# Kernel optimization log

Hardware: AMD Instinct MI355X
Metric: run time of the kernel (lower is better)

Reference implementation:

```python
import jax, jax.numpy as jnp
import numpy as np

B, S, D, H, F, REF = 4, 1024, 512, 8, 2048, 2
HGRID = 32   # sqrt(seq_len)
HALF = 3     # 7x7 window -> half-width 3


def _masks():
    i = jnp.arange(HGRID)
    near = jnp.abs(i[:, None] - i[None, :]) <= HALF            # [h,h]
    inside = (near[:, None, :, None] & near[None, :, None, :]).reshape(S, S)
    # reverse=True mask (mca): outside-window -> -inf, inside -> 0
    m_rev = jnp.where(inside, 0.0, -jnp.inf).astype(jnp.float32)
    # reverse=False mask (msa/nsa): inside-window -> -inf, outside -> 0 (faithful to source)
    m_fwd = jnp.where(inside, -jnp.inf, 0.0).astype(jnp.float32)
    return m_rev, m_fwd


def _mha(q, k, v, w, b, ow, ob, mask):
    # torch nn.MultiheadAttention, batch_first, eval mode (no dropout)
    hd = D // H
    wq, wk, wv = jnp.split(w, 3, axis=0)
    bq, bk, bv = jnp.split(b, 3)

    def proj(t, wt, bt):
        Bt, Lt = t.shape[0], t.shape[1]
        return (t @ wt.T + bt).reshape(Bt, Lt, H, hd).transpose(0, 2, 1, 3)

    qh, kh, vh = proj(q, wq, bq), proj(k, wk, bk), proj(v, wv, bv)
    scores = jnp.einsum('bhqd,bhkd->bhqk', qh, kh) / jnp.sqrt(jnp.float32(hd))
    if mask is not None:
        scores = scores + mask
    a = jax.nn.softmax(scores, axis=-1)
    o = jnp.einsum('bhqk,bhkd->bhqd', a, vh).transpose(0, 2, 1, 3).reshape(q.shape[0], q.shape[1], D)
    return o @ ow.T + ob


def _ln(x, g, b, eps=1e-5):
    m = x.mean(-1, keepdims=True)
    v = ((x - m) ** 2).mean(-1, keepdims=True)
    return (x - m) / jnp.sqrt(v + eps) * g + b


def setup_inputs() -> dict:
    key = jax.random.key(0)
    ks = jax.random.split(key, 16)
    d = {}
    d['x'] = jax.random.normal(ks[0], (B, S, D), jnp.float32)
    d['ref_mca'] = jax.random.normal(ks[1], (B, REF * S, D), jnp.float32)
    d['gate'] = jax.random.uniform(ks[2], (B, S, 5), jnp.float32)
    i = 3
    for p in ['mca', 'ca', 'msa', 'nsa', 'sa']:
        d[p + '_w'] = 0.02 * jax.random.normal(ks[i], (3 * D, D), jnp.float32); i += 1
        d[p + '_b'] = jnp.zeros((3 * D,), jnp.float32)
        d[p + '_ow'] = 0.02 * jax.random.normal(ks[i], (D, D), jnp.float32); i += 1
        d[p + '_ob'] = jnp.zeros((D,), jnp.float32)
    d['ln1_g'] = jnp.ones((D,), jnp.float32); d['ln1_b'] = jnp.zeros((D,), jnp.float32)
    d['ln2_g'] = jnp.ones((D,), jnp.float32); d['ln2_b'] = jnp.zeros((D,), jnp.float32)
    d['fc1_w'] = 0.02 * jax.random.normal(ks[i], (F, D), jnp.float32); i += 1
    d['fc1_b'] = jnp.zeros((F,), jnp.float32)
    d['fc2_w'] = 0.02 * jax.random.normal(ks[i], (D, F), jnp.float32); i += 1
    d['fc2_b'] = jnp.zeros((D,), jnp.float32)
    return d


def reference(x, ref_mca, gate,
              mca_w, mca_b, mca_ow, mca_ob,
              ca_w, ca_b, ca_ow, ca_ob,
              msa_w, msa_b, msa_ow, msa_ob,
              nsa_w, nsa_b, nsa_ow, nsa_ob,
              sa_w, sa_b, sa_ow, sa_ob,
              ln1_g, ln1_b, ln2_g, ln2_b,
              fc1_w, fc1_b, fc2_w, fc2_b):
    m_rev, m_fwd = _masks()
    # mca branch: sum attention over each seq_len chunk of ref_mca (window-inside mask)
    mca_x = jnp.zeros_like(x)
    for r in range(REF):
        chunk = ref_mca[:, r * S:(r + 1) * S, :]
        mca_x = mca_x + _mha(x, chunk, chunk, mca_w, mca_b, mca_ow, mca_ob, m_rev)
    # faithful to source: loop variable leaks, so ca/nsa use the LAST chunk
    ref_last = ref_mca[:, (REF - 1) * S:, :]
    new_x = gate[:, :, 0:1] * mca_x
    new_x = new_x + gate[:, :, 1:2] * _mha(x, ref_last, ref_last, ca_w, ca_b, ca_ow, ca_ob, None)
    new_x = new_x + gate[:, :, 2:3] * _mha(x, x, x, msa_w, msa_b, msa_ow, msa_ob, m_fwd)
    new_x = new_x + gate[:, :, 3:4] * _mha(x, ref_last, x, nsa_w, nsa_b, nsa_ow, nsa_ob, m_fwd)
    new_x = new_x + gate[:, :, 4:5] * _mha(x, x, x, sa_w, sa_b, sa_ow, sa_ob, None)
    h = _ln(new_x, ln1_g, ln1_b)
    y = jax.nn.gelu(h @ fc1_w.T + fc1_b, approximate=False) @ fc2_w.T + fc2_b
    return _ln(h + y, ln2_g, ln2_b)
```

## Files before the change

### kernel.cpp

```cpp
#include <hip/hip_runtime.h>

typedef __bf16 bf16_t;
typedef bf16_t bf16x8 __attribute__((ext_vector_type(8)));
typedef float f32x4v __attribute__((ext_vector_type(4)));
typedef unsigned int u32;
typedef unsigned long long u64;

__device__ __forceinline__ void gload16(const bf16_t* g, bf16_t* l) {
    __builtin_amdgcn_global_load_lds((const __attribute__((address_space(1))) u32*)g,
                                     (__attribute__((address_space(3))) u32*)l, 16, 0, 0);
}

#define QSCALE 0.18033688011112042f

struct PackBDesc {
    int nseg;
    int blkOf[21];
    const float* src[20];
    bf16_t* dst[20];
    int chunks[20];
    int dstLd[20];
    int shift[20];
};

__global__ __launch_bounds__(256) void packb_k(PackBDesc d) {
    int b = blockIdx.x;
    int s = 0;
    while (s + 1 < d.nseg && b >= d.blkOf[s + 1]) ++s;
    int idx = (b - d.blkOf[s]) * 256 + threadIdx.x;
    if (idx >= d.chunks[s]) return;
    const float* src = d.src[s] + (size_t)idx * 8;
    int r = idx >> d.shift[s];
    int c8 = idx & ((1 << d.shift[s]) - 1);
    bf16_t* dst = d.dst[s] + (size_t)r * d.dstLd[s] + (size_t)c8 * 8;
    float4 v0 = reinterpret_cast<const float4*>(src)[0];
    float4 v1 = reinterpret_cast<const float4*>(src)[1];
    bf16x8 o;
    o[0] = (bf16_t)v0.x; o[1] = (bf16_t)v0.y; o[2] = (bf16_t)v0.z; o[3] = (bf16_t)v0.w;
    o[4] = (bf16_t)v1.x; o[5] = (bf16_t)v1.y; o[6] = (bf16_t)v1.z; o[7] = (bf16_t)v1.w;
    *reinterpret_cast<bf16x8*>(dst) = o;
}

struct PackFDesc {
    int nseg;
    int blkOf[15];
    const float* src[14];
    float* dst[14];
    int n[14];
};

__global__ __launch_bounds__(256) void packf_k(PackFDesc d) {
    int b = blockIdx.x;
    int s = 0;
    while (s + 1 < d.nseg && b >= d.blkOf[s + 1]) ++s;
    int idx = (b - d.blkOf[s]) * 256 + threadIdx.x;
    if (idx >= d.n[s]) return;
    d.dst[s][idx] = d.src[s][idx];
}

template <int EPI, int BM, int BN>
__device__ __forceinline__ void gemm_core(
    int tm, int tn, int bz,
    const bf16_t* __restrict__ A, int aBS, int aRowOff, int lda,
    const bf16_t* __restrict__ B,
    const float* __restrict__ bias,
    void* __restrict__ Out, int ldo, size_t outSplitStride,
    const float* __restrict__ gate, const float* __restrict__ obcat,
    int kStart, int kLen, u64 scaleMask) {
    constexpr int MB = BM / 32, NB = BN / 32, WM = BM / 2, WN = BN / 2;
    constexpr int CA = BM / 64, CB = BN / 64;
    __shared__ __attribute__((aligned(16))) bf16_t As[2][BM * 32];
    __shared__ __attribute__((aligned(16))) bf16_t Bs[2][BN * 32];
    const int tid = threadIdx.x, lane = tid & 63, w = tid >> 6;
    const int wm = w >> 1, wn = w & 1;
    const int l15 = lane & 15, l16 = lane >> 4;
    const int colS = (lane & 3) * 8, rowS = lane >> 2;

    auto remap = [&](int m) { return (m >> 10) * aBS + aRowOff + (m & 1023); };

    const bf16_t* aS[CA];
    const bf16_t* bS[CB];
#pragma unroll
    for (int c = 0; c < CA; ++c)
        aS[c] = A + (size_t)remap(tm * BM + (CA * w + c) * 16 + rowS) * lda + kStart + colS;
#pragma unroll
    for (int c = 0; c < CB; ++c)
        bS[c] = B + (size_t)(tn * BN + (CB * w + c) * 16 + rowS) * lda + kStart + colS;

    auto stage = [&](int buf, int t) {
        const size_t o = (size_t)t * 32;
#pragma unroll
        for (int c = 0; c < CA; ++c) gload16(aS[c] + o, &As[buf][(CA * w + c) * 512]);
#pragma unroll
        for (int c = 0; c < CB; ++c) gload16(bS[c] + o, &Bs[buf][(CB * w + c) * 512]);
    };

    f32x4v acc[MB][NB] = {};
    const int nt = kLen / 32;
    stage(0, 0);
    __syncthreads();
    int cur = 0;
    for (int t = 0; t < nt; ++t) {
        if (t + 1 < nt) stage(cur ^ 1, t + 1);
        bf16x8 af[MB], bff[NB];
#pragma unroll
        for (int mi = 0; mi < MB; ++mi)
            af[mi] = *reinterpret_cast<const bf16x8*>(&As[cur][(wm * WM + mi * 16 + l15) * 32 + l16 * 8]);
#pragma unroll
        for (int ni = 0; ni < NB; ++ni)
            bff[ni] = *reinterpret_cast<const bf16x8*>(&Bs[cur][(wn * WN + ni * 16 + l15) * 32 + l16 * 8]);
#pragma unroll
        for (int mi = 0; mi < MB; ++mi)
#pragma unroll
            for (int ni = 0; ni < NB; ++ni)
                acc[mi][ni] = __builtin_amdgcn_mfma_f32_16x16x32_bf16(af[mi], bff[ni], acc[mi][ni], 0, 0, 0);
        __syncthreads();
        cur ^= 1;
    }

    const bool doScale = (EPI == 0) && ((scaleMask >> tn) & 1ULL);
#pragma unroll
    for (int mi = 0; mi < MB; ++mi) {
#pragma unroll
        for (int ni = 0; ni < NB; ++ni) {
#pragma unroll
            for (int i = 0; i < 4; ++i) {
                int row = tm * BM + wm * WM + mi * 16 + l16 * 4 + i;
                int n = tn * BN + wn * WN + ni * 16 + l15;
                float v = acc[mi][ni][i];
                if (bias && bz == 0) v += bias[n];
                if constexpr (EPI == 0) {
                    if (doScale) v *= QSCALE;
                    ((bf16_t*)Out)[(size_t)row * ldo + n] = (bf16_t)v;
                } else if constexpr (EPI == 1) {
                    float g = 0.5f * v * (1.0f + erff(v * 0.70710678118654752f));
                    ((bf16_t*)Out)[(size_t)row * ldo + n] = (bf16_t)g;
                } else if constexpr (EPI == 3) {
                    ((float*)Out + (size_t)bz * outSplitStride)[(size_t)row * ldo + n] = v;
                } else {
                    if (obcat && bz == 0) {
#pragma unroll
                        for (int p = 0; p < 5; ++p) {
                            float c = (p == 0) ? 2.0f : 1.0f;
                            v += gate[row * 5 + p] * c * obcat[p * 512 + n];
                        }
                    }
                    ((float*)Out + (size_t)bz * outSplitStride)[(size_t)row * ldo + n] = v;
                }
            }
        }
    }
}

struct ProjDesc {
    const bf16_t* A[3];
    int aBS[3], aRowOff[3];
    const bf16_t* B[3];
    const float* bias[3];
    bf16_t* Out[3];
    int ldo[3];
    int ntn[3], base[3];
    u64 qmask[3];
};

__global__ __launch_bounds__(256) void proj_k(ProjDesc d) {
    int wg = (blockIdx.x & 7) * 272 + (blockIdx.x >> 3);
    int s = (wg >= d.base[2]) ? 2 : (wg >= d.base[1]) ? 1 : 0;
    int local = wg - d.base[s];
    int tn = local % d.ntn[s];
    int tm = local / d.ntn[s];
    gemm_core<0, 128, 128>(tm, tn, 0, d.A[s], d.aBS[s], d.aRowOff[s], 512,
                           d.B[s], d.bias[s], d.Out[s], d.ldo[s], 0, nullptr, nullptr, 0, 512,
                           d.qmask[s]);
}

template <int EPI, int BM, int BN>
__global__ __launch_bounds__(256) void gemmT(
    const bf16_t* __restrict__ A, int aBS, int aRowOff, int lda,
    const bf16_t* __restrict__ B, const float* __restrict__ bias,
    void* __restrict__ Out, int ldo, size_t outSplitStride,
    const float* __restrict__ gate, const float* __restrict__ obcat, int kPerSplit) {
    gemm_core<EPI, BM, BN>(blockIdx.y, blockIdx.x, blockIdx.z, A, aBS, aRowOff, lda, B, bias,
                           Out, ldo, outSplitStride, gate, obcat, blockIdx.z * kPerSplit, kPerSplit, 0);
}

struct AttnDesc {
    const bf16_t* Q[6];
    const bf16_t* K[6];
    const bf16_t* V[6];
    int ldq[6], ldk[6], ldv[6];
    int segOff[6], gidx[6], mask[6];
    bf16_t* acat;
    bf16_t* Op;
    float* Mp;
    float* Lp;
    const float* gate;
};

__global__ __launch_bounds__(512) void attn5_k(AttnDesc d) {
    __shared__ __attribute__((aligned(16))) bf16_t Ks[64][72];
    __shared__ __attribute__((aligned(16))) bf16_t Vt[64][72];
    __shared__ __attribute__((aligned(16))) bf16_t Ps[8][16][40];

    int bid = blockIdx.x;
    int g = bid % 320;
    int qt = bid / 320;
    int u, lg;
    if (g < 32) { u = 0; lg = g; }
    else if (g < 64) { u = 1; lg = g - 32; }
    else if (g < 128) { u = 2; lg = g - 64; }
    else if (g < 192) { u = 3; lg = g - 128; }
    else if (g < 256) { u = 4; lg = g - 192; }
    else { u = 5; lg = g - 256; }
    const bool splitk = (u >= 2);
    const int mask = d.mask[u];
    const int h = lg & 7, z = lg >> 3;
    int b, split;
    if (splitk) { b = z & 3; split = z >> 2; } else { b = z; split = 0; }

    const int tid = threadIdx.x;
    const int lane = tid & 63;
    const int w = tid >> 6;
    const int l15 = lane & 15, l16 = lane >> 4;

    const int qr = qt * 128 + w * 16;
    const int qrow = b * 1024 + qr;
    const int qblk = qr >> 5;
    const int qg = ((w & 1) * 16) + l15;

    const int ldq = d.ldq[u], ldk = d.ldk[u], ldv = d.ldv[u];
    bf16x8 aq[2];
#pragma unroll
    for (int s = 0; s < 2; ++s)
        aq[s] = *reinterpret_cast<const bf16x8*>(
            d.Q[u] + (size_t)(qrow + l15) * ldq + h * 64 + s * 32 + l16 * 8);

    float mrow = -1e30f, lsum = 0.f;
    f32x4v accO[4] = {};

    const int srow = tid >> 3, scol8 = (tid & 7) * 8;
    const int vcol = srow ^ ((tid & 7) << 3);
    const bf16_t* kbase = d.K[u] + (size_t)(b * 1024) * ldk + h * 64 + scol8;
    const bf16_t* vbase = d.V[u] + (size_t)(b * 1024) * ldv + h * 64 + scol8;

    int t0, t1;
    if (splitk) { t0 = split * 8; t1 = t0 + 8; }
    else {
        int klo = qt * 4 - 3; if (klo < 0) klo = 0;
        int khi = qt * 4 + 6; if (khi > 31) khi = 31;
        t0 = klo >> 1; t1 = (khi >> 1) + 1;
    }

    bf16x8 rk, rv, rk2, rv2;
    rk = *reinterpret_cast<const bf16x8*>(kbase + (size_t)(t0 * 64 + srow) * ldk);
    rv = *reinterpret_cast<const bf16x8*>(vbase + (size_t)(t0 * 64 + srow) * ldv);

    for (int tt = t0; tt < t1; ++tt) {
        __syncthreads();
        *reinterpret_cast<bf16x8*>(&Ks[srow][scol8]) = rk;
#pragma unroll
        for (int j = 0; j < 8; ++j) Vt[scol8 + j][vcol] = rv[j];
        if (tt + 1 < t1) {
            rk2 = *reinterpret_cast<const bf16x8*>(kbase + (size_t)((tt + 1) * 64 + srow) * ldk);
            rv2 = *reinterpret_cast<const bf16x8*>(vbase + (size_t)((tt + 1) * 64 + srow) * ldv);
        }
        __syncthreads();

        int bd0 = qblk - tt * 2;     if (bd0 < 0) bd0 = -bd0;
        int bd1 = qblk - tt * 2 - 1; if (bd1 < 0) bd1 = -bd1;
        const bool a0 = (mask != 1) || (bd0 <= 3);
        const bool a1 = (mask != 1) || (bd1 <= 3);
        if (a0 || a1) {
            f32x4v z4[4];
#pragma unroll
            for (int nt = 0; nt < 4; ++nt) {
                bf16x8 kf0 = *reinterpret_cast<const bf16x8*>(&Ks[nt * 16 + l15][l16 * 8]);
                bf16x8 kf1 = *reinterpret_cast<const bf16x8*>(&Ks[nt * 16 + l15][32 + l16 * 8]);
                f32x4v zz = {};
                zz = __builtin_amdgcn_mfma_f32_16x16x32_bf16(kf0, aq[0], zz, 0, 0, 0);
                zz = __builtin_amdgcn_mfma_f32_16x16x32_bf16(kf1, aq[1], zz, 0, 0, 0);
                z4[nt] = zz;
            }
            float p[4][4];
#pragma unroll
            for (int nt = 0; nt < 4; ++nt) {
                const int bd = (nt >> 1) ? bd1 : bd0;
                const bool act = (nt >> 1) ? a1 : a0;
                const bool needMask = (mask == 1) || (mask == 2 && bd <= 3);
#pragma unroll
                for (int i = 0; i < 4; ++i) {
                    float v = z4[nt][i];
                    if (!act) v = -1e30f;
                    else if (needMask) {
                        int k5 = (nt & 1) * 16 + l16 * 4 + i;
                        int dq = qg - k5; if (dq < 0) dq = -dq;
                        bool inside = (bd <= 3) && (dq <= 3);
                        if (mask == 1 ? !inside : inside) v = -1e30f;
                    }
                    p[nt][i] = v;
                }
            }
            float tmx = p[0][0];
#pragma unroll
            for (int nt = 0; nt < 4; ++nt)
#pragma unroll
                for (int i = 0; i < 4; ++i) tmx = fmaxf(tmx, p[nt][i]);
            tmx = fmaxf(tmx, __shfl_xor(tmx, 16, 64));
            tmx = fmaxf(tmx, __shfl_xor(tmx, 32, 64));
            if (!__all(tmx - mrow <= 8.0f)) {
                float mn = fmaxf(mrow, tmx);
                float fac = exp2f(mrow - mn);
                mrow = mn;
                lsum *= fac;
                float facq[4];
#pragma unroll
                for (int i = 0; i < 4; ++i) facq[i] = __shfl(fac, l16 * 4 + i, 64);
#pragma unroll
                for (int dblk = 0; dblk < 4; ++dblk)
#pragma unroll
                    for (int i = 0; i < 4; ++i) accO[dblk][i] *= facq[i];
            }
            float rs = 0.f;
#pragma unroll
            for (int nt = 0; nt < 4; ++nt)
#pragma unroll
                for (int i = 0; i < 4; ++i) {
                    p[nt][i] = exp2f(p[nt][i] - mrow);
                    rs += p[nt][i];
                }
            rs += __shfl_xor(rs, 16, 64);
            rs += __shfl_xor(rs, 32, 64);
            lsum += rs;

#pragma unroll
            for (int kh = 0; kh < 2; ++kh) {
#pragma unroll
                for (int n = 0; n < 2; ++n)
#pragma unroll
                    for (int i = 0; i < 4; ++i)
                        Ps[w][l15][n * 16 + l16 * 4 + i] = (bf16_t)p[kh * 2 + n][i];
                bf16x8 pa = *reinterpret_cast<const bf16x8*>(&Ps[w][l15][l16 * 8]);
#pragma unroll
                for (int dblk = 0; dblk < 4; ++dblk) {
                    int dd = dblk * 16 + l15;
                    int csw = ((kh * 4 + l16) ^ (dd >> 3)) * 8;
                    bf16x8 bv = *reinterpret_cast<const bf16x8*>(&Vt[dd][csw]);
                    accO[dblk] = __builtin_amdgcn_mfma_f32_16x16x32_bf16(pa, bv, accO[dblk], 0, 0, 0);
                }
            }
        }
        rk = rk2; rv = rv2;
    }

    if (!splitk) {
        float inv = 1.0f / lsum;
        float invq[4];
#pragma unroll
        for (int i = 0; i < 4; ++i) invq[i] = __shfl(inv, l16 * 4 + i, 64);
#pragma unroll
        for (int dblk = 0; dblk < 4; ++dblk)
#pragma unroll
            for (int i = 0; i < 4; ++i) {
                float gg = d.gate[(size_t)(qrow + l16 * 4 + i) * 5 + d.gidx[u]];
                d.acat[(size_t)(qrow + l16 * 4 + i) * 3072 + d.segOff[u] + h * 64 + dblk * 16 + l15] =
                    (bf16_t)(accO[dblk][i] * invq[i] * gg);
            }
    } else {
        const int su = u - 2;
        bf16_t* Opu = d.Op + (size_t)su * 65536 * 64;
        float* Mpu = d.Mp + su * 65536;
        float* Lpu = d.Lp + su * 65536;
        int pb = ((split * 4 + b) * 8 + h) * 1024 + qr;
        if (l16 == 0) { Mpu[pb + l15] = mrow; Lpu[pb + l15] = lsum; }
#pragma unroll
        for (int dblk = 0; dblk < 4; ++dblk)
#pragma unroll
            for (int i = 0; i < 4; ++i) {
                float gg = d.gate[(size_t)(qrow + l16 * 4 + i) * 5 + d.gidx[u]];
                Opu[(size_t)(pb + l16 * 4 + i) * 64 + dblk * 16 + l15] = (bf16_t)(accO[dblk][i] * gg);
            }
    }
}

struct MergeDesc {
    const bf16_t* Op;
    const float* Mp;
    const float* Lp;
    bf16_t* acat;
    int segOff[4];
};

__global__ __launch_bounds__(256) void merge4_k(MergeDesc d) {
    int u = blockIdx.x >> 10;
    int idx = (blockIdx.x & 1023) * 256 + threadIdx.x;
    const bf16_t* Opu = d.Op + (size_t)u * 65536 * 64;
    const float* Mpu = d.Mp + u * 65536;
    const float* Lpu = d.Lp + u * 65536;
    int dg = idx & 7;
    int q = (idx >> 3) & 1023;
    int h = (idx >> 13) & 7;
    int b = idx >> 16;
    int r0 = ((0 * 4 + b) * 8 + h) * 1024 + q;
    int r1 = ((1 * 4 + b) * 8 + h) * 1024 + q;
    float m0 = Mpu[r0], m1 = Mpu[r1], l0 = Lpu[r0], l1 = Lpu[r1];
    float M = fmaxf(m0, m1);
    float w0 = exp2f(m0 - M), w1 = exp2f(m1 - M);
    float den = 1.0f / (l0 * w0 + l1 * w1);
    bf16x8 o0 = *reinterpret_cast<const bf16x8*>(Opu + (size_t)r0 * 64 + dg * 8);
    bf16x8 o1 = *reinterpret_cast<const bf16x8*>(Opu + (size_t)r1 * 64 + dg * 8);
    bf16x8 o;
#pragma unroll
    for (int j = 0; j < 8; ++j)
        o[j] = (bf16_t)(((float)o0[j] * w0 + (float)o1[j] * w1) * den);
    *reinterpret_cast<bf16x8*>(d.acat + (size_t)(b * 1024 + q) * 3072 + d.segOff[u] + h * 64 + dg * 8) = o;
}

__global__ __launch_bounds__(256) void ln_k(const float* __restrict__ in0,
                                            const float* __restrict__ in1,
                                            const float* __restrict__ in2,
                                            const float* __restrict__ g,
                                            const float* __restrict__ bb,
                                            float* __restrict__ outf,
                                            bf16_t* __restrict__ outb) {
    __shared__ float red[8];
    int row = blockIdx.x;
    int t = threadIdx.x;
    float x0 = in0[(size_t)row * 512 + t];
    float x1 = in0[(size_t)row * 512 + 256 + t];
    if (in1) {
        x0 += in1[(size_t)row * 512 + t];
        x1 += in1[(size_t)row * 512 + 256 + t];
    }
    if (in2) {
        x0 += in2[(size_t)row * 512 + t];
        x1 += in2[(size_t)row * 512 + 256 + t];
    }
    float s = x0 + x1, sq = x0 * x0 + x1 * x1;
#pragma unroll
    for (int d = 1; d < 64; d <<= 1) {
        s += __shfl_xor(s, d, 64);
        sq += __shfl_xor(sq, d, 64);
    }
    int w = t >> 6;
    if ((t & 63) == 0) { red[w] = s; red[4 + w] = sq; }
    __syncthreads();
    s = red[0] + red[1] + red[2] + red[3];
    sq = red[4] + red[5] + red[6] + red[7];
    float mean = s * (1.0f / 512.0f);
    float var = sq * (1.0f / 512.0f) - mean * mean;
    float rstd = rsqrtf(var + 1e-5f);
    float y0 = (x0 - mean) * rstd * g[t] + bb[t];
    float y1 = (x1 - mean) * rstd * g[256 + t] + bb[256 + t];
    if (outf) {
        outf[(size_t)row * 512 + t] = y0;
        outf[(size_t)row * 512 + 256 + t] = y1;
    }
    if (outb) {
        outb[(size_t)row * 512 + t] = (bf16_t)y0;
        outb[(size_t)row * 512 + 256 + t] = (bf16_t)y1;
    }
}

extern "C" void kernel_launch(void* const* d_in, const int* in_sizes, int n_in,
                              void* d_out, int out_size, void* d_ws, size_t ws_size,
                              hipStream_t stream) {
    (void)in_sizes; (void)n_in; (void)out_size; (void)ws_size;
    const float* x       = (const float*)d_in[0];
    const float* ref_mca = (const float*)d_in[1];
    const float* gate    = (const float*)d_in[2];
    const float *w[5], *wb[5], *ow[5], *ob[5];
    for (int p = 0; p < 5; ++p) {
        w[p]  = (const float*)d_in[3 + p * 4];
        wb[p] = (const float*)d_in[4 + p * 4];
        ow[p] = (const float*)d_in[5 + p * 4];
        ob[p] = (const float*)d_in[6 + p * 4];
    }
    const float* ln1_g = (const float*)d_in[23];
    const float* ln1_b = (const float*)d_in[24];
    const float* ln2_g = (const float*)d_in[25];
    const float* ln2_b = (const float*)d_in[26];
    const float* fc1_w = (const float*)d_in[27];
    const float* fc1_b = (const float*)d_in[28];
    const float* fc2_w = (const float*)d_in[29];
    const float* fc2_b = (const float*)d_in[30];

    char* ws = (char*)d_ws;
    size_t off = 0;
    auto alloc = [&](size_t bytes) {
        char* p = ws + off;
        off += (bytes + 255) & ~(size_t)255;
        return p;
    };
    const size_t S2 = (size_t)4096 * 512;
    bf16_t* xb    = (bf16_t*)alloc(S2 * 2);
    bf16_t* refb  = (bf16_t*)alloc((size_t)8192 * 512 * 2);
    bf16_t* Wxp   = (bf16_t*)alloc((size_t)5120 * 512 * 2);
    bf16_t* WRp   = (bf16_t*)alloc((size_t)2560 * 512 * 2);
    bf16_t* Wop   = (bf16_t*)alloc((size_t)512 * 3072 * 2);
    bf16_t* fc1p  = (bf16_t*)alloc((size_t)2048 * 512 * 2);
    bf16_t* fc2p  = (bf16_t*)alloc((size_t)512 * 2048 * 2);
    float*  bxp   = (float*)alloc((size_t)5120 * 4);
    float*  brp   = (float*)alloc((size_t)2560 * 4);
    float*  obc   = (float*)alloc((size_t)5 * 512 * 4);
    bf16_t* XP    = (bf16_t*)alloc((size_t)4096 * 5120 * 2);
    bf16_t* RP    = (bf16_t*)alloc((size_t)4096 * 2560 * 2);
    bf16_t* R0    = (bf16_t*)alloc((size_t)4096 * 1024 * 2);
    bf16_t* acat  = (bf16_t*)alloc((size_t)4096 * 3072 * 2);
    float*  newx  = (float*)alloc(S2 * 4 * 2);
    float*  hbuf  = (float*)alloc(S2 * 4);
    bf16_t* Opart = (bf16_t*)alloc((size_t)4 * 65536 * 64 * 2);
    float*  Mpart = (float*)alloc((size_t)4 * 65536 * 4);
    float*  Lpart = (float*)alloc((size_t)4 * 65536 * 4);
    bf16_t* hb  = refb;
    bf16_t* ub  = XP;
    float*  yp  = newx;

    PackBDesc pb{};
    int nb = 0, blk = 0;
    auto addB = [&](const float* s, bf16_t* dptr, int chunks, int dstLd, int shift) {
        pb.src[nb] = s; pb.dst[nb] = dptr; pb.chunks[nb] = chunks;
        pb.dstLd[nb] = dstLd; pb.shift[nb] = shift;
        pb.blkOf[nb] = blk; blk += (chunks + 255) / 256; ++nb;
    };
    auto addLin = [&](const float* s, bf16_t* dptr, long elems) {
        addB(s, dptr, (int)(elems / 8), 0, 30);
    };
    addLin(x, xb, (long)4096 * 512);
    addLin(ref_mca, refb, (long)8192 * 512);
    addLin(w[0], Wxp, (long)512 * 512);
    addLin(w[1], Wxp + (size_t)512 * 512, (long)512 * 512);
    addLin(w[2], Wxp + (size_t)1024 * 512, (long)1536 * 512);
    addLin(w[3], Wxp + (size_t)2560 * 512, (long)512 * 512);
    addLin(w[3] + (size_t)1024 * 512, Wxp + (size_t)3072 * 512, (long)512 * 512);
    addLin(w[4], Wxp + (size_t)3584 * 512, (long)1536 * 512);
    addLin(w[0] + (size_t)512 * 512, WRp, (long)1024 * 512);
    addLin(w[1] + (size_t)512 * 512, WRp + (size_t)1024 * 512, (long)1024 * 512);
    addLin(w[3] + (size_t)512 * 512, WRp + (size_t)2048 * 512, (long)512 * 512);
    const float* owSeg[6] = {ow[0], ow[0], ow[1], ow[2], ow[3], ow[4]};
    for (int s = 0; s < 6; ++s)
        addB(owSeg[s], Wop + (size_t)s * 512, 32768, 3072, 6);
    addLin(fc1_w, fc1p, (long)2048 * 512);
    addLin(fc2_w, fc2p, (long)512 * 2048);
    pb.nseg = nb; pb.blkOf[nb] = blk;
    packb_k<<<blk, 256, 0, stream>>>(pb);

    PackFDesc pf{};
    int nf = 0, fblk = 0;
    auto addF = [&](const float* s, float* dptr, int n) {
        pf.src[nf] = s; pf.dst[nf] = dptr; pf.n[nf] = n;
        pf.blkOf[nf] = fblk; fblk += (n + 255) / 256; ++nf;
    };
    addF(wb[0], bxp, 512);
    addF(wb[1], bxp + 512, 512);
    addF(wb[2], bxp + 1024, 1536);
    addF(wb[3], bxp + 2560, 512);
    addF(wb[3] + 1024, bxp + 3072, 512);
    addF(wb[4], bxp + 3584, 1536);
    addF(wb[0] + 512, brp, 1024);
    addF(wb[1] + 512, brp + 1024, 1024);
    addF(wb[3] + 512, brp + 2048, 512);
    for (int p = 0; p < 5; ++p) addF(ob[p], obc + p * 512, 512);
    pf.nseg = nf; pf.blkOf[nf] = fblk;
    packf_k<<<fblk, 256, 0, stream>>>(pf);

    ProjDesc pd{};
    pd.A[0] = xb;   pd.aBS[0] = 1024; pd.aRowOff[0] = 0;    pd.B[0] = Wxp; pd.bias[0] = bxp; pd.Out[0] = XP; pd.ldo[0] = 5120; pd.ntn[0] = 40;
    pd.A[1] = refb; pd.aBS[1] = 2048; pd.aRowOff[1] = 1024; pd.B[1] = WRp; pd.bias[1] = brp; pd.Out[1] = RP; pd.ldo[1] = 2560; pd.ntn[1] = 20;
    pd.A[2] = refb; pd.aBS[2] = 2048; pd.aRowOff[2] = 0;    pd.B[2] = WRp; pd.bias[2] = brp; pd.Out[2] = R0; pd.ldo[2] = 1024; pd.ntn[2] = 8;
    pd.base[0] = 0; pd.base[1] = 40 * 32; pd.base[2] = 40 * 32 + 20 * 32;
    pd.qmask[0] = 0xF0F00FFFULL; pd.qmask[1] = 0; pd.qmask[2] = 0;
    proj_k<<<(40 + 20 + 8) * 32, 256, 0, stream>>>(pd);

    AttnDesc ad{};
    auto setU = [&](int u, const bf16_t* Q, int lq, const bf16_t* K, int lk,
                    const bf16_t* V, int lv, int seg, int gi, int mk) {
        ad.Q[u] = Q; ad.ldq[u] = lq; ad.K[u] = K; ad.ldk[u] = lk; ad.V[u] = V; ad.ldv[u] = lv;
        ad.segOff[u] = seg; ad.gidx[u] = gi; ad.mask[u] = mk;
    };
    setU(0, XP, 5120, R0, 1024, R0 + 512, 1024, 0, 0, 1);
    setU(1, XP, 5120, RP, 2560, RP + 512, 2560, 512, 0, 1);
    setU(2, XP + 512, 5120, RP + 1024, 2560, RP + 1536, 2560, 1024, 1, 0);
    setU(3, XP + 1024, 5120, XP + 1536, 5120, XP + 2048, 5120, 1536, 2, 2);
    setU(4, XP + 2560, 5120, RP + 2048, 2560, XP + 3072, 5120, 2048, 3, 2);
    setU(5, XP + 3584, 5120, XP + 4096, 5120, XP + 4608, 5120, 2560, 4, 0);
    ad.acat = acat; ad.Op = Opart; ad.Mp = Mpart; ad.Lp = Lpart; ad.gate = gate;
    attn5_k<<<2560, 512, 0, stream>>>(ad);

    MergeDesc md{};
    md.Op = Opart; md.Mp = Mpart; md.Lp = Lpart; md.acat = acat;
    md.segOff[0] = 1024; md.segOff[1] = 1536; md.segOff[2] = 2048; md.segOff[3] = 2560;
    merge4_k<<<4096, 256, 0, stream>>>(md);

    gemmT<4, 64, 64><<<dim3(8, 64, 2), 256, 0, stream>>>(acat, 1024, 0, 3072, Wop, nullptr,
                                                         newx, 512, S2, gate, obc, 1536);
    ln_k<<<4096, 256, 0, stream>>>(newx, newx + S2, nullptr, ln1_g, ln1_b, hbuf, hb);
    gemmT<1, 128, 128><<<dim3(16, 32, 1), 256, 0, stream>>>(hb, 1024, 0, 512, fc1p, fc1_b,
                                                            ub, 2048, 0, nullptr, nullptr, 512);
    gemmT<3, 64, 64><<<dim3(8, 64, 2), 256, 0, stream>>>(ub, 1024, 0, 2048, fc2p, fc2_b,
                                                         yp, 512, S2, nullptr, nullptr, 1024);
    ln_k<<<4096, 256, 0, stream>>>(hbuf, yp, yp + S2, ln2_g, ln2_b, (float*)d_out, nullptr);
}
```

Measured before the change: 320.5 us.

## Restructure attention: 32 query rows per wave, drop split-K and merge kernel

The attention kernel now processes two 16-row query tiles per wave (256 rows per block), so each staged K/V tile is reused across twice as many queries. The split-K path for unmasked and forward-masked units is removed along with its partial buffers and the separate merge kernel; each block walks the full key range itself. Block indices are remapped so blocks interleave across XCDs, and launch bounds request 4 waves per SIMD. The grid drops from 2560 to 768 blocks, which lowers parallelism and raises register pressure per thread in exchange for less K/V traffic, no partial writes and one fewer launch.

```diff
diff --git a/kernel.cpp b/kernel.cpp
--- a/kernel.cpp
+++ b/kernel.cpp
@@ -191,52 +191,43 @@
     int ldq[6], ldk[6], ldv[6];
     int segOff[6], gidx[6], mask[6];
     bf16_t* acat;
-    bf16_t* Op;
-    float* Mp;
-    float* Lp;
     const float* gate;
 };
 
-__global__ __launch_bounds__(512) void attn5_k(AttnDesc d) {
+__global__ __launch_bounds__(512, 4) void attn6_k(AttnDesc d) {
     __shared__ __attribute__((aligned(16))) bf16_t Ks[64][72];
     __shared__ __attribute__((aligned(16))) bf16_t Vt[64][72];
-    __shared__ __attribute__((aligned(16))) bf16_t Ps[8][16][40];
-
-    int bid = blockIdx.x;
-    int g = bid % 320;
-    int qt = bid / 320;
-    int u, lg;
-    if (g < 32) { u = 0; lg = g; }
-    else if (g < 64) { u = 1; lg = g - 32; }
-    else if (g < 128) { u = 2; lg = g - 64; }
-    else if (g < 192) { u = 3; lg = g - 128; }
-    else if (g < 256) { u = 4; lg = g - 192; }
-    else { u = 5; lg = g - 256; }
-    const bool splitk = (u >= 2);
+    __shared__ __attribute__((aligned(16))) bf16_t Ps[8][2][16][40];
+
+    const int bid = blockIdx.x;
+    const int xcd = bid & 7;
+    const int qt = (bid >> 3) & 3;
+    const int gg = bid >> 5;
+    const int g = gg * 8 + xcd;
+    const int u = g >> 5, lg = g & 31;
     const int mask = d.mask[u];
-    const int h = lg & 7, z = lg >> 3;
-    int b, split;
-    if (splitk) { b = z & 3; split = z >> 2; } else { b = z; split = 0; }
+    const int h = lg & 7, b = lg >> 3;
 
     const int tid = threadIdx.x;
     const int lane = tid & 63;
     const int w = tid >> 6;
     const int l15 = lane & 15, l16 = lane >> 4;
 
-    const int qr = qt * 128 + w * 16;
-    const int qrow = b * 1024 + qr;
-    const int qblk = qr >> 5;
-    const int qg = ((w & 1) * 16) + l15;
-
+    const int qbase = qt * 256 + w * 32;
+    const int qrow = b * 1024 + qbase;
+    const int qblk = qbase >> 5;
     const int ldq = d.ldq[u], ldk = d.ldk[u], ldv = d.ldv[u];
-    bf16x8 aq[2];
-#pragma unroll
-    for (int s = 0; s < 2; ++s)
-        aq[s] = *reinterpret_cast<const bf16x8*>(
-            d.Q[u] + (size_t)(qrow + l15) * ldq + h * 64 + s * 32 + l16 * 8);
-
-    float mrow = -1e30f, lsum = 0.f;
-    f32x4v accO[4] = {};
+
+    bf16x8 aq[2][2];
+#pragma unroll
+    for (int t = 0; t < 2; ++t)
+#pragma unroll
+        for (int s = 0; s < 2; ++s)
+            aq[t][s] = *reinterpret_cast<const bf16x8*>(
+                d.Q[u] + (size_t)(qrow + t * 16 + l15) * ldq + h * 64 + s * 32 + l16 * 8);
+
+    float mrow0 = -1e30f, mrow1 = -1e30f, lsum0 = 0.f, lsum1 = 0.f;
+    f32x4v accO[2][4] = {};
 
     const int srow = tid >> 3, scol8 = (tid & 7) * 8;
     const int vcol = srow ^ ((tid & 7) << 3);
@@ -244,12 +235,11 @@
     const bf16_t* vbase = d.V[u] + (size_t)(b * 1024) * ldv + h * 64 + scol8;
 
     int t0, t1;
-    if (splitk) { t0 = split * 8; t1 = t0 + 8; }
-    else {
-        int klo = qt * 4 - 3; if (klo < 0) klo = 0;
-        int khi = qt * 4 + 6; if (khi > 31) khi = 31;
+    if (mask == 1) {
+        int klo = qt * 8 - 3;  if (klo < 0) klo = 0;
+        int khi = qt * 8 + 10; if (khi > 31) khi = 31;
         t0 = klo >> 1; t1 = (khi >> 1) + 1;
-    }
+    } else { t0 = 0; t1 = 16; }
 
     bf16x8 rk, rv, rk2, rv2;
     rk = *reinterpret_cast<const bf16x8*>(kbase + (size_t)(t0 * 64 + srow) * ldk);
@@ -271,148 +261,129 @@
         const bool a0 = (mask != 1) || (bd0 <= 3);
         const bool a1 = (mask != 1) || (bd1 <= 3);
         if (a0 || a1) {
-            f32x4v z4[4];
+            f32x4v z[2][4];
 #pragma unroll
             for (int nt = 0; nt < 4; ++nt) {
                 bf16x8 kf0 = *reinterpret_cast<const bf16x8*>(&Ks[nt * 16 + l15][l16 * 8]);
                 bf16x8 kf1 = *reinterpret_cast<const bf16x8*>(&Ks[nt * 16 + l15][32 + l16 * 8]);
-                f32x4v zz = {};
-                zz = __builtin_amdgcn_mfma_f32_16x16x32_bf16(kf0, aq[0], zz, 0, 0, 0);
-                zz = __builtin_amdgcn_mfma_f32_16x16x32_bf16(kf1, aq[1], zz, 0, 0, 0);
-                z4[nt] = zz;
+                f32x4v z0 = {}, z1 = {};
+                z0 = __builtin_amdgcn_mfma_f32_16x16x32_bf16(kf0, aq[0][0], z0, 0, 0, 0);
+                z0 = __builtin_amdgcn_mfma_f32_16x16x32_bf16(kf1, aq[0][1], z0, 0, 0, 0);
+                z1 = __builtin_amdgcn_mfma_f32_16x16x32_bf16(kf0, aq[1][0], z1, 0, 0, 0);
+                z1 = __builtin_amdgcn_mfma_f32_16x16x32_bf16(kf1, aq[1][1], z1, 0, 0, 0);
+                z[0][nt] = z0; z[1][nt] = z1;
             }
-            float p[4][4];
-#pragma unroll
-            for (int nt = 0; nt < 4; ++nt) {
-                const int bd = (nt >> 1) ? bd1 : bd0;
-                const bool act = (nt >> 1) ? a1 : a0;
-                const bool needMask = (mask == 1) || (mask == 2 && bd <= 3);
-#pragma unroll
-                for (int i = 0; i < 4; ++i) {
-                    float v = z4[nt][i];
-                    if (!act) v = -1e30f;
-                    else if (needMask) {
-                        int k5 = (nt & 1) * 16 + l16 * 4 + i;
-                        int dq = qg - k5; if (dq < 0) dq = -dq;
-                        bool inside = (bd <= 3) && (dq <= 3);
-                        if (mask == 1 ? !inside : inside) v = -1e30f;
+            float p[2][4][4];
+#pragma unroll
+            for (int t = 0; t < 2; ++t) {
+                const int qgt = t * 16 + l15;
+#pragma unroll
+                for (int nt = 0; nt < 4; ++nt) {
+                    const int bd = (nt >> 1) ? bd1 : bd0;
+                    const bool act = (nt >> 1) ? a1 : a0;
+                    const bool needMask = (mask == 1) || (mask == 2 && bd <= 3);
+#pragma unroll
+                    for (int i = 0; i < 4; ++i) {
+                        float v = z[t][nt][i];
+                        if (!act) v = -1e30f;
+                        else if (needMask) {
+                            int k5 = (nt & 1) * 16 + l16 * 4 + i;
+                            int dq = qgt - k5; if (dq < 0) dq = -dq;
+                            bool inside = (bd <= 3) && (dq <= 3);
+                            if (mask == 1 ? !inside : inside) v = -1e30f;
+                        }
+                        p[t][nt][i] = v;
                     }
-                    p[nt][i] = v;
                 }
             }
-            float tmx = p[0][0];
+            float tmx0 = p[0][0][0], tmx1 = p[1][0][0];
 #pragma unroll
             for (int nt = 0; nt < 4; ++nt)
 #pragma unroll
-                for (int i = 0; i < 4; ++i) tmx = fmaxf(tmx, p[nt][i]);
-            tmx = fmaxf(tmx, __shfl_xor(tmx, 16, 64));
-            tmx = fmaxf(tmx, __shfl_xor(tmx, 32, 64));
-            if (!__all(tmx - mrow <= 8.0f)) {
-                float mn = fmaxf(mrow, tmx);
-                float fac = exp2f(mrow - mn);
-                mrow = mn;
-                lsum *= fac;
-                float facq[4];
-#pragma unroll
-                for (int i = 0; i < 4; ++i) facq[i] = __shfl(fac, l16 * 4 + i, 64);
+                for (int i = 0; i < 4; ++i) {
+                    tmx0 = fmaxf(tmx0, p[0][nt][i]);
+                    tmx1 = fmaxf(tmx1, p[1][nt][i]);
+                }
+            tmx0 = fmaxf(tmx0, __shfl_xor(tmx0, 16, 64));
+            tmx0 = fmaxf(tmx0, __shfl_xor(tmx0, 32, 64));
+            tmx1 = fmaxf(tmx1, __shfl_xor(tmx1, 16, 64));
+            tmx1 = fmaxf(tmx1, __shfl_xor(tmx1, 32, 64));
+            float grow = fmaxf(tmx0 - mrow0, tmx1 - mrow1);
+            if (!__all(grow <= 8.0f)) {
+                float mn0 = fmaxf(mrow0, tmx0), mn1 = fmaxf(mrow1, tmx1);
+                float f0 = exp2f(mrow0 - mn0), f1 = exp2f(mrow1 - mn1);
+                mrow0 = mn0; mrow1 = mn1;
+                lsum0 *= f0; lsum1 *= f1;
+                float fq0[4], fq1[4];
+#pragma unroll
+                for (int i = 0; i < 4; ++i) {
+                    fq0[i] = __shfl(f0, l16 * 4 + i, 64);
+                    fq1[i] = __shfl(f1, l16 * 4 + i, 64);
+                }
 #pragma unroll
                 for (int dblk = 0; dblk < 4; ++dblk)
 #pragma unroll
-                    for (int i = 0; i < 4; ++i) accO[dblk][i] *= facq[i];
+                    for (int i = 0; i < 4; ++i) {
+                        accO[0][dblk][i] *= fq0[i];
+                        accO[1][dblk][i] *= fq1[i];
+                    }
             }
-            float rs = 0.f;
+            float rs0 = 0.f, rs1 = 0.f;
 #pragma unroll
             for (int nt = 0; nt < 4; ++nt)
 #pragma unroll
                 for (int i = 0; i < 4; ++i) {
-                    p[nt][i] = exp2f(p[nt][i] - mrow);
-                    rs += p[nt][i];
+                    p[0][nt][i] = exp2f(p[0][nt][i] - mrow0); rs0 += p[0][nt][i];
+                    p[1][nt][i] = exp2f(p[1][nt][i] - mrow1); rs1 += p[1][nt][i];
                 }
-            rs += __shfl_xor(rs, 16, 64);
-            rs += __shfl_xor(rs, 32, 64);
-            lsum += rs;
+            rs0 += __shfl_xor(rs0, 16, 64); rs0 += __shfl_xor(rs0, 32, 64);
+            rs1 += __shfl_xor(rs1, 16, 64); rs1 += __shfl_xor(rs1, 32, 64);
+            lsum0 += rs0; lsum1 += rs1;
 
 #pragma unroll
             for (int kh = 0; kh < 2; ++kh) {
 #pragma unroll
                 for (int n = 0; n < 2; ++n)
 #pragma unroll
-                    for (int i = 0; i < 4; ++i)
-                        Ps[w][l15][n * 16 + l16 * 4 + i] = (bf16_t)p[kh * 2 + n][i];
-                bf16x8 pa = *reinterpret_cast<const bf16x8*>(&Ps[w][l15][l16 * 8]);
+                    for (int i = 0; i < 4; ++i) {
+                        Ps[w][0][l15][n * 16 + l16 * 4 + i] = (bf16_t)p[0][kh * 2 + n][i];
+                        Ps[w][1][l15][n * 16 + l16 * 4 + i] = (bf16_t)p[1][kh * 2 + n][i];
+                    }
+                bf16x8 pa0 = *reinterpret_cast<const bf16x8*>(&Ps[w][0][l15][l16 * 8]);
+                bf16x8 pa1 = *reinterpret_cast<const bf16x8*>(&Ps[w][1][l15][l16 * 8]);
 #pragma unroll
                 for (int dblk = 0; dblk < 4; ++dblk) {
                     int dd = dblk * 16 + l15;
                     int csw = ((kh * 4 + l16) ^ (dd >> 3)) * 8;
                     bf16x8 bv = *reinterpret_cast<const bf16x8*>(&Vt[dd][csw]);
-                    accO[dblk] = __builtin_amdgcn_mfma_f32_16x16x32_bf16(pa, bv, accO[dblk], 0, 0, 0);
+                    accO[0][dblk] = __builtin_amdgcn_mfma_f32_16x16x32_bf16(pa0, bv, accO[0][dblk], 0, 0, 0);
+                    accO[1][dblk] = __builtin_amdgcn_mfma_f32_16x16x32_bf16(pa1, bv, accO[1][dblk], 0, 0, 0);
                 }
             }
         }
         rk = rk2; rv = rv2;
     }
 
-    if (!splitk) {
-        float inv = 1.0f / lsum;
-        float invq[4];
-#pragma unroll
-        for (int i = 0; i < 4; ++i) invq[i] = __shfl(inv, l16 * 4 + i, 64);
-#pragma unroll
-        for (int dblk = 0; dblk < 4; ++dblk)
-#pragma unroll
-            for (int i = 0; i < 4; ++i) {
-                float gg = d.gate[(size_t)(qrow + l16 * 4 + i) * 5 + d.gidx[u]];
-                d.acat[(size_t)(qrow + l16 * 4 + i) * 3072 + d.segOff[u] + h * 64 + dblk * 16 + l15] =
-                    (bf16_t)(accO[dblk][i] * invq[i] * gg);
-            }
-    } else {
-        const int su = u - 2;
-        bf16_t* Opu = d.Op + (size_t)su * 65536 * 64;
-        float* Mpu = d.Mp + su * 65536;
-        float* Lpu = d.Lp + su * 65536;
-        int pb = ((split * 4 + b) * 8 + h) * 1024 + qr;
-        if (l16 == 0) { Mpu[pb + l15] = mrow; Lpu[pb + l15] = lsum; }
-#pragma unroll
-        for (int dblk = 0; dblk < 4; ++dblk)
-#pragma unroll
-            for (int i = 0; i < 4; ++i) {
-                float gg = d.gate[(size_t)(qrow + l16 * 4 + i) * 5 + d.gidx[u]];
-                Opu[(size_t)(pb + l16 * 4 + i) * 64 + dblk * 16 + l15] = (bf16_t)(accO[dblk][i] * gg);
-            }
-    }
-}
-
-struct MergeDesc {
-    const bf16_t* Op;
-    const float* Mp;
-    const float* Lp;
-    bf16_t* acat;
-    int segOff[4];
-};
-
-__global__ __launch_bounds__(256) void merge4_k(MergeDesc d) {
-    int u = blockIdx.x >> 10;
-    int idx = (blockIdx.x & 1023) * 256 + threadIdx.x;
-    const bf16_t* Opu = d.Op + (size_t)u * 65536 * 64;
-    const float* Mpu = d.Mp + u * 65536;
-    const float* Lpu = d.Lp + u * 65536;
-    int dg = idx & 7;
-    int q = (idx >> 3) & 1023;
-    int h = (idx >> 13) & 7;
-    int b = idx >> 16;
-    int r0 = ((0 * 4 + b) * 8 + h) * 1024 + q;
-    int r1 = ((1 * 4 + b) * 8 + h) * 1024 + q;
-    float m0 = Mpu[r0], m1 = Mpu[r1], l0 = Lpu[r0], l1 = Lpu[r1];
-    float M = fmaxf(m0, m1);
-    float w0 = exp2f(m0 - M), w1 = exp2f(m1 - M);
-    float den = 1.0f / (l0 * w0 + l1 * w1);
-    bf16x8 o0 = *reinterpret_cast<const bf16x8*>(Opu + (size_t)r0 * 64 + dg * 8);
-    bf16x8 o1 = *reinterpret_cast<const bf16x8*>(Opu + (size_t)r1 * 64 + dg * 8);
-    bf16x8 o;
-#pragma unroll
-    for (int j = 0; j < 8; ++j)
-        o[j] = (bf16_t)(((float)o0[j] * w0 + (float)o1[j] * w1) * den);
-    *reinterpret_cast<bf16x8*>(d.acat + (size_t)(b * 1024 + q) * 3072 + d.segOff[u] + h * 64 + dg * 8) = o;
+    float inv0 = 1.0f / lsum0, inv1 = 1.0f / lsum1;
+    float iq0[4], iq1[4];
+#pragma unroll
+    for (int i = 0; i < 4; ++i) {
+        iq0[i] = __shfl(inv0, l16 * 4 + i, 64);
+        iq1[i] = __shfl(inv1, l16 * 4 + i, 64);
+    }
+#pragma unroll
+    for (int dblk = 0; dblk < 4; ++dblk)
+#pragma unroll
+        for (int i = 0; i < 4; ++i) {
+            int r0 = qrow + l16 * 4 + i;
+            int r1 = r0 + 16;
+            float g0 = d.gate[(size_t)r0 * 5 + d.gidx[u]];
+            float g1 = d.gate[(size_t)r1 * 5 + d.gidx[u]];
+            d.acat[(size_t)r0 * 3072 + d.segOff[u] + h * 64 + dblk * 16 + l15] =
+                (bf16_t)(accO[0][dblk][i] * iq0[i] * g0);
+            d.acat[(size_t)r1 * 3072 + d.segOff[u] + h * 64 + dblk * 16 + l15] =
+                (bf16_t)(accO[1][dblk][i] * iq1[i] * g1);
+        }
 }
 
 __global__ __launch_bounds__(256) void ln_k(const float* __restrict__ in0,
@@ -508,9 +479,6 @@
     bf16_t* acat  = (bf16_t*)alloc((size_t)4096 * 3072 * 2);
     float*  newx  = (float*)alloc(S2 * 4 * 2);
     float*  hbuf  = (float*)alloc(S2 * 4);
-    bf16_t* Opart = (bf16_t*)alloc((size_t)4 * 65536 * 64 * 2);
-    float*  Mpart = (float*)alloc((size_t)4 * 65536 * 4);
-    float*  Lpart = (float*)alloc((size_t)4 * 65536 * 4);
     bf16_t* hb  = refb;
     bf16_t* ub  = XP;
     float*  yp  = newx;
@@ -583,13 +551,8 @@
     setU(3, XP + 1024, 5120, XP + 1536, 5120, XP + 2048, 5120, 1536, 2, 2);
     setU(4, XP + 2560, 5120, RP + 2048, 2560, XP + 3072, 5120, 2048, 3, 2);
     setU(5, XP + 3584, 5120, XP + 4096, 5120, XP + 4608, 5120, 2560, 4, 0);
-    ad.acat = acat; ad.Op = Opart; ad.Mp = Mpart; ad.Lp = Lpart; ad.gate = gate;
-    attn5_k<<<2560, 512, 0, stream>>>(ad);
-
-    MergeDesc md{};
-    md.Op = Opart; md.Mp = Mpart; md.Lp = Lpart; md.acat = acat;
-    md.segOff[0] = 1024; md.segOff[1] = 1536; md.segOff[2] = 2048; md.segOff[3] = 2560;
-    merge4_k<<<4096, 256, 0, stream>>>(md);
+    ad.acat = acat; ad.gate = gate;
+    attn6_k<<<768, 512, 0, stream>>>(ad);
 
     gemmT<4, 64, 64><<<dim3(8, 64, 2), 256, 0, stream>>>(acat, 1024, 0, 3072, Wop, nullptr,
                                                          newx, 512, S2, gate, obc, 1536);
```

New measurement: 313.1 us (median of 2 runs). 2.3% less time.
